# Performance work log

Measured on AMD Instinct MI355X. Metric: run time of the kernel, lower is better.

## Reference

```python
import jax, jax.numpy as jnp
import numpy as np

DECAY = 0.8
CODEBOOK_SIZE = 1024
DIM = 128


def setup_inputs() -> dict:
    key = jax.random.key(0)
    k1, k2 = jax.random.split(key)
    x = jax.random.normal(k1, (16, 4096, DIM), dtype=jnp.float32)
    embed = jax.random.normal(k2, (CODEBOOK_SIZE, DIM), dtype=jnp.float32)
    ema_embed = embed * 1.0  # ema_num_initial = 1.0
    ema_num = jnp.ones((CODEBOOK_SIZE,), dtype=jnp.float32)
    return {"x": x, "embed": embed, "ema_embed": ema_embed, "ema_num": ema_num}


def reference(x, embed, ema_embed, ema_num):
    # flatten: [..., d] -> [N, d]
    shape = x.shape
    flatten = x.reshape(-1, shape[-1])  # [N, d]
    distance = -2.0 * (flatten @ embed.T) + jnp.sum(embed * embed, axis=-1)  # [N, K]
    embed_ind = jnp.argmin(distance, axis=-1)  # [N]
    quantize = embed[embed_ind.reshape(shape[:-1])]  # gather -> [..., d]

    # training branch: onehot^T @ flatten == segment_sum over code indices
    num_curr = jax.ops.segment_sum(
        jnp.ones_like(embed_ind, dtype=jnp.float32), embed_ind,
        num_segments=CODEBOOK_SIZE)  # [K]
    embed_curr = jax.ops.segment_sum(
        flatten.astype(jnp.float32), embed_ind,
        num_segments=CODEBOOK_SIZE)  # [K, d]

    ema_num_new = ema_num * DECAY + (1.0 - DECAY) * num_curr
    ema_embed_new = ema_embed * DECAY + (1.0 - DECAY) * embed_curr
    embed_new = ema_embed_new / ema_num_new[:, None]
    return quantize, embed_new, ema_embed_new, ema_num_new
```

## Files before the change

### kernel.cpp

```cpp
#include <hip/hip_runtime.h>

#define NPTS    65536
#define DIM     128
#define KCODES  1024
#define BM      64
#define TILE_C  64
#define NTHR    256
#define NTILE   (KCODES / TILE_C)

typedef _Float16 f16x8 __attribute__((ext_vector_type(8)));
typedef float    f32x4 __attribute__((ext_vector_type(4)));

__device__ __forceinline__ void gload_lds16(const void* g, void* l) {
    __builtin_amdgcn_global_load_lds(
        (const __attribute__((address_space(1))) void*)g,
        (__attribute__((address_space(3))) void*)l, 16, 0, 0);
}

__global__ __launch_bounds__(256)
void pack_kernel(const float* __restrict__ embed, _Float16* __restrict__ ebf,
                 int* __restrict__ ghist, const float* __restrict__ ema_embed,
                 float* __restrict__ acc, float* __restrict__ hn)
{
    __shared__ float partial[256];
    const int t = threadIdx.x;
    const int b = blockIdx.x;
    const int g = b * 256 + t;
    if (g < KCODES) ghist[g] = 0;
    {
        float4 e0 = reinterpret_cast<const float4*>(ema_embed)[g];
        float4 e1 = reinterpret_cast<const float4*>(ema_embed)[g + 16384];
        reinterpret_cast<float4*>(acc)[g] =
            (float4){0.8f * e0.x, 0.8f * e0.y, 0.8f * e0.z, 0.8f * e0.w};
        reinterpret_cast<float4*>(acc)[g + 16384] =
            (float4){0.8f * e1.x, 0.8f * e1.y, 0.8f * e1.z, 0.8f * e1.w};
    }

    const int tc  = g >> 10;
    const int f   = (g >> 6) & 15;
    const int l   = g & 63;
    const int nt  = f >> 2;
    const int akk = f & 3;
    const int hg  = l >> 4;
    const int n   = l & 15;
    const int c   = tc * TILE_C + nt * 16 + n;
    const int d0  = akk * 32 + hg * 8;
    const float* src = embed + (long)c * DIM + d0;
    float4 v0 = *reinterpret_cast<const float4*>(src);
    float4 v1 = *reinterpret_cast<const float4*>(src + 4);
    float vv[8] = {v0.x, v0.y, v0.z, v0.w, v1.x, v1.y, v1.z, v1.w};
    f16x8 out;
    float ss = 0.f;
    #pragma unroll
    for (int j = 0; j < 8; ++j) {
        _Float16 h = (_Float16)vv[j];
        out[j] = h;
        float r = (float)h;
        ss += r * r;
    }
    *reinterpret_cast<f16x8*>(ebf + (long)g * 8) = out;

    partial[t] = ss;
    __syncthreads();
    if (t < 16) {
        float s = 0.f;
        #pragma unroll
        for (int k = 0; k < 16; ++k) s += partial[t + k * 16];
        hn[(b >> 2) * TILE_C + (b & 3) * 16 + t] = 0.5f * s;
    }
}

__global__ __launch_bounds__(NTHR, 4)
void argmin_kernel(const float* __restrict__ x, const _Float16* __restrict__ ebf,
                   const float* __restrict__ halfnorm, const float* __restrict__ embed,
                   float* __restrict__ quant, int* __restrict__ ghist,
                   float* __restrict__ acc)
{
    __shared__ _Float16 es[2][8192];
    __shared__ int      hist[KCODES];
    __shared__ int      bidx[BM];

    const int t    = threadIdx.x;
    const int lane = t & 63;
    const int w    = t >> 6;
    const int r16  = lane & 15;
    const int h4   = lane >> 4;
    const long xbase = (long)blockIdx.x * BM * DIM;
    const int  wp    = w * 16;

    for (int i = t; i < KCODES; i += NTHR) hist[i] = 0;

    f16x8 a[4];
    {
        const long prow = xbase + (long)(wp + r16) * DIM;
        #pragma unroll
        for (int akk = 0; akk < 4; ++akk) {
            const float* s = x + prow + akk * 32 + h4 * 8;
            float4 u0 = *reinterpret_cast<const float4*>(s);
            float4 u1 = *reinterpret_cast<const float4*>(s + 4);
            float vv[8] = {u0.x, u0.y, u0.z, u0.w, u1.x, u1.y, u1.z, u1.w};
            #pragma unroll
            for (int j = 0; j < 8; ++j) a[akk][j] = (_Float16)vv[j];
        }
    }

    #pragma unroll
    for (int i = 0; i < 4; ++i) {
        const int f = w * 4 + i;
        gload_lds16(ebf + (long)f * 512 + lane * 8, &es[0][f * 512]);
    }
    float hnv_cur[4], hnv_nxt[4];
    #pragma unroll
    for (int nt = 0; nt < 4; ++nt) hnv_cur[nt] = halfnorm[nt * 16 + r16];
    __syncthreads();

    float bestv[4];
    int   besti[4];
    #pragma unroll
    for (int s = 0; s < 4; ++s) { bestv[s] = -1e30f; besti[s] = 0; }

    #pragma unroll 1
    for (int tile = 0; tile < NTILE; ++tile) {
        if (tile + 1 < NTILE) {
            const long gbase = (long)(tile + 1) * 8192;
            #pragma unroll
            for (int i = 0; i < 4; ++i) {
                const int f = w * 4 + i;
                gload_lds16(ebf + gbase + f * 512 + lane * 8, &es[(tile + 1) & 1][f * 512]);
            }
            #pragma unroll
            for (int nt = 0; nt < 4; ++nt)
                hnv_nxt[nt] = halfnorm[(tile + 1) * TILE_C + nt * 16 + r16];
        }

        f32x4 C[4];
        #pragma unroll
        for (int nt = 0; nt < 4; ++nt) C[nt] = (f32x4){0.f, 0.f, 0.f, 0.f};

        #pragma unroll
        for (int akk = 0; akk < 4; ++akk) {
            #pragma unroll
            for (int nt = 0; nt < 4; ++nt) {
                f16x8 B = *reinterpret_cast<const f16x8*>(
                    &es[tile & 1][(nt * 4 + akk) * 512 + lane * 8]);
                C[nt] = __builtin_amdgcn_mfma_f32_16x16x32_f16(a[akk], B, C[nt], 0, 0, 0);
            }
        }

        #pragma unroll
        for (int nt = 0; nt < 4; ++nt) {
            const int c = tile * TILE_C + nt * 16 + r16;
            #pragma unroll
            for (int reg = 0; reg < 4; ++reg) {
                float sc = C[nt][reg] - hnv_cur[nt];
                if (sc > bestv[reg]) { bestv[reg] = sc; besti[reg] = c; }
            }
        }
        #pragma unroll
        for (int nt = 0; nt < 4; ++nt) hnv_cur[nt] = hnv_nxt[nt];
        __syncthreads();
    }

    #pragma unroll
    for (int s = 0; s < 4; ++s) {
        float v = bestv[s];
        int   i = besti[s];
        #pragma unroll
        for (int off = 1; off < 16; off <<= 1) {
            float ov = __shfl_xor(v, off);
            int   oi = __shfl_xor(i, off);
            if (ov > v || (ov == v && oi < i)) { v = ov; i = oi; }
        }
        bestv[s] = v; besti[s] = i;
    }
    if (r16 == 0) {
        #pragma unroll
        for (int s = 0; s < 4; ++s) {
            int p = wp + h4 * 4 + s;
            bidx[p] = besti[s];
        }
    }
    __syncthreads();

    if (t < BM) atomicAdd(&hist[bidx[t]], 1);

    float4* dst = reinterpret_cast<float4*>(quant + xbase);
    #pragma unroll
    for (int i = 0; i < 8; ++i) {
        int idx = i * NTHR + t;
        int p   = idx >> 5;
        int q   = idx & 31;
        int c   = bidx[p];
        dst[idx] = reinterpret_cast<const float4*>(embed + (long)c * DIM)[q];
    }

    __syncthreads();
    for (int i = t; i < KCODES; i += NTHR)
        if (hist[i]) atomicAdd(&ghist[i], hist[i]);

    #pragma unroll 4
    for (int rep = 0; rep < BM * DIM / NTHR; ++rep) {
        const int flat = rep * NTHR + t;
        const int p    = flat >> 7;
        const int d    = flat & 127;
        atomicAdd(&acc[(long)bidx[p] * DIM + d],
                  0.2f * x[xbase + (long)p * DIM + d]);
    }
}

__global__ __launch_bounds__(256)
void final_kernel(const float* __restrict__ acc, const int* __restrict__ ghist,
                  const float* __restrict__ ema_num, float* __restrict__ ema_num_new,
                  float* __restrict__ embed_new)
{
    const int g = blockIdx.x * 256 + threadIdx.x;
    const int c = g >> 5;
    float4 v = reinterpret_cast<const float4*>(acc)[g];
    const float en = ema_num[c] * 0.8f + 0.2f * (float)ghist[c];
    if ((g & 31) == 0) ema_num_new[c] = en;
    float4 o = {v.x / en, v.y / en, v.z / en, v.w / en};
    reinterpret_cast<float4*>(embed_new)[g] = o;
}

extern "C" void kernel_launch(void* const* d_in, const int* in_sizes, int n_in,
                              void* d_out, int out_size, void* d_ws, size_t ws_size,
                              hipStream_t stream)
{
    const float* x         = (const float*)d_in[0];
    const float* embed     = (const float*)d_in[1];
    const float* ema_embed = (const float*)d_in[2];
    const float* ema_num   = (const float*)d_in[3];

    float* out0 = (float*)d_out;
    float* out1 = out0 + 8388608;
    float* out2 = out1 + 131072;
    float* out3 = out2 + 131072;

    char* ws = (char*)d_ws;
    float*    hn    = (float*)ws;
    _Float16* ebf   = (_Float16*)(ws + 4096);
    int*      ghist = (int*)(ws + 266240);

    pack_kernel<<<64, 256, 0, stream>>>(embed, ebf, ghist, ema_embed, out2, hn);
    argmin_kernel<<<NPTS / BM, NTHR, 0, stream>>>(x, ebf, hn, embed, out0, ghist, out2);
    final_kernel<<<128, 256, 0, stream>>>(out2, ghist, ema_num, out3, out1);
}
```

Baseline: 119.8 us.

## Replace global atomic scatter with per-code gather kernel over stored indices

```diff
diff --git a/kernel.cpp b/kernel.cpp
--- a/kernel.cpp
+++ b/kernel.cpp
@@ -19,22 +19,12 @@
 
 __global__ __launch_bounds__(256)
 void pack_kernel(const float* __restrict__ embed, _Float16* __restrict__ ebf,
-                 int* __restrict__ ghist, const float* __restrict__ ema_embed,
-                 float* __restrict__ acc, float* __restrict__ hn)
+                 float* __restrict__ hn)
 {
     __shared__ float partial[256];
     const int t = threadIdx.x;
     const int b = blockIdx.x;
     const int g = b * 256 + t;
-    if (g < KCODES) ghist[g] = 0;
-    {
-        float4 e0 = reinterpret_cast<const float4*>(ema_embed)[g];
-        float4 e1 = reinterpret_cast<const float4*>(ema_embed)[g + 16384];
-        reinterpret_cast<float4*>(acc)[g] =
-            (float4){0.8f * e0.x, 0.8f * e0.y, 0.8f * e0.z, 0.8f * e0.w};
-        reinterpret_cast<float4*>(acc)[g + 16384] =
-            (float4){0.8f * e1.x, 0.8f * e1.y, 0.8f * e1.z, 0.8f * e1.w};
-    }
 
     const int tc  = g >> 10;
     const int f   = (g >> 6) & 15;
@@ -72,13 +62,9 @@
 
 __global__ __launch_bounds__(NTHR, 4)
 void argmin_kernel(const float* __restrict__ x, const _Float16* __restrict__ ebf,
-                   const float* __restrict__ halfnorm, const float* __restrict__ embed,
-                   float* __restrict__ quant, int* __restrict__ ghist,
-                   float* __restrict__ acc)
+                   const float* __restrict__ halfnorm, int* __restrict__ ind)
 {
     __shared__ _Float16 es[2][8192];
-    __shared__ int      hist[KCODES];
-    __shared__ int      bidx[BM];
 
     const int t    = threadIdx.x;
     const int lane = t & 63;
@@ -88,8 +74,6 @@
     const long xbase = (long)blockIdx.x * BM * DIM;
     const int  wp    = w * 16;
 
-    for (int i = t; i < KCODES; i += NTHR) hist[i] = 0;
-
     f16x8 a[4];
     {
         const long prow = xbase + (long)(wp + r16) * DIM;
@@ -177,49 +161,61 @@
         #pragma unroll
         for (int s = 0; s < 4; ++s) {
             int p = wp + h4 * 4 + s;
-            bidx[p] = besti[s];
-        }
-    }
+            ind[blockIdx.x * BM + p] = besti[s];
+        }
+    }
+}
+
+__global__ __launch_bounds__(256)
+void codesum_kernel(const float* __restrict__ x, const int* __restrict__ ind,
+                    const float* __restrict__ embed, const float* __restrict__ ema_embed,
+                    const float* __restrict__ ema_num, float* __restrict__ quant,
+                    float* __restrict__ embed_new, float* __restrict__ ema_embed_new,
+                    float* __restrict__ ema_num_new)
+{
+    __shared__ float wacc[4][DIM];
+    __shared__ int   wcnt[4];
+    const int c    = blockIdx.x;
+    const int t    = threadIdx.x;
+    const int lane = t & 63;
+    const int w    = t >> 6;
+
+    for (int i = t; i < 4 * DIM; i += 256) (&wacc[0][0])[i] = 0.f;
+
+    const float er0 = embed[(long)c * DIM + lane];
+    const float er1 = embed[(long)c * DIM + 64 + lane];
+
+    int cnt = 0;
+    const int base = w * (NPTS / 4);
+    #pragma unroll 1
+    for (int k = 0; k < NPTS / 4; k += 64) {
+        const int v = ind[base + k + lane];
+        cnt += (v == c) ? 1 : 0;
+        unsigned long long m = __ballot(v == c);
+        while (m) {
+            const int l = __ffsll((unsigned long long)m) - 1;
+            m &= m - 1;
+            const long p = base + k + l;
+            wacc[w][lane]      += x[p * DIM + lane];
+            wacc[w][lane + 64] += x[p * DIM + 64 + lane];
+            quant[p * DIM + lane]      = er0;
+            quant[p * DIM + 64 + lane] = er1;
+        }
+    }
+    #pragma unroll
+    for (int off = 32; off > 0; off >>= 1) cnt += __shfl_xor(cnt, off);
+    if (lane == 0) wcnt[w] = cnt;
     __syncthreads();
 
-    if (t < BM) atomicAdd(&hist[bidx[t]], 1);
-
-    float4* dst = reinterpret_cast<float4*>(quant + xbase);
-    #pragma unroll
-    for (int i = 0; i < 8; ++i) {
-        int idx = i * NTHR + t;
-        int p   = idx >> 5;
-        int q   = idx & 31;
-        int c   = bidx[p];
-        dst[idx] = reinterpret_cast<const float4*>(embed + (long)c * DIM)[q];
-    }
-
-    __syncthreads();
-    for (int i = t; i < KCODES; i += NTHR)
-        if (hist[i]) atomicAdd(&ghist[i], hist[i]);
-
-    #pragma unroll 4
-    for (int rep = 0; rep < BM * DIM / NTHR; ++rep) {
-        const int flat = rep * NTHR + t;
-        const int p    = flat >> 7;
-        const int d    = flat & 127;
-        atomicAdd(&acc[(long)bidx[p] * DIM + d],
-                  0.2f * x[xbase + (long)p * DIM + d]);
-    }
-}
-
-__global__ __launch_bounds__(256)
-void final_kernel(const float* __restrict__ acc, const int* __restrict__ ghist,
-                  const float* __restrict__ ema_num, float* __restrict__ ema_num_new,
-                  float* __restrict__ embed_new)
-{
-    const int g = blockIdx.x * 256 + threadIdx.x;
-    const int c = g >> 5;
-    float4 v = reinterpret_cast<const float4*>(acc)[g];
-    const float en = ema_num[c] * 0.8f + 0.2f * (float)ghist[c];
-    if ((g & 31) == 0) ema_num_new[c] = en;
-    float4 o = {v.x / en, v.y / en, v.z / en, v.w / en};
-    reinterpret_cast<float4*>(embed_new)[g] = o;
+    if (t < DIM) {
+        const float n  = (float)(wcnt[0] + wcnt[1] + wcnt[2] + wcnt[3]);
+        const float en = ema_num[c] * 0.8f + 0.2f * n;
+        const float s  = wacc[0][t] + wacc[1][t] + wacc[2][t] + wacc[3][t];
+        const float ee = ema_embed[(long)c * DIM + t] * 0.8f + 0.2f * s;
+        ema_embed_new[(long)c * DIM + t] = ee;
+        embed_new[(long)c * DIM + t]     = ee / en;
+        if (t == 0) ema_num_new[c] = en;
+    }
 }
 
 extern "C" void kernel_launch(void* const* d_in, const int* in_sizes, int n_in,
@@ -237,11 +233,12 @@
     float* out3 = out2 + 131072;
 
     char* ws = (char*)d_ws;
-    float*    hn    = (float*)ws;
-    _Float16* ebf   = (_Float16*)(ws + 4096);
-    int*      ghist = (int*)(ws + 266240);
-
-    pack_kernel<<<64, 256, 0, stream>>>(embed, ebf, ghist, ema_embed, out2, hn);
-    argmin_kernel<<<NPTS / BM, NTHR, 0, stream>>>(x, ebf, hn, embed, out0, ghist, out2);
-    final_kernel<<<128, 256, 0, stream>>>(out2, ghist, ema_num, out3, out1);
-}
+    float*    hn  = (float*)ws;
+    _Float16* ebf = (_Float16*)(ws + 4096);
+    int*      ind = (int*)(ws + 266240);
+
+    pack_kernel<<<64, 256, 0, stream>>>(embed, ebf, hn);
+    argmin_kernel<<<NPTS / BM, NTHR, 0, stream>>>(x, ebf, hn, ind);
+    codesum_kernel<<<KCODES, 256, 0, stream>>>(x, ind, embed, ema_embed, ema_num,
+                                               out0, out1, out2, out3);
+}
```

Result: slower. 282.2 us (+135.6%).
